# Optimization experiments

Measured on AMD Instinct MI355X. Metric: run time of the kernel, lower is better.

## Reference

```python
import jax, jax.numpy as jnp
import numpy as np

G, R, M, H, NH, OUT = 2048, 1024, 1024, 256, 8, 2
DH = H // NH


def _ln(x, g, b):
    m = jnp.mean(x, -1, keepdims=True)
    v = jnp.var(x, -1, keepdims=True)
    return (x - m) * jax.lax.rsqrt(v + 1e-5) * g + b


def _mha(xq, xkv, w, mask=None):
    # w: [4, H, H] = (Wq, Wk, Wv, Wo); mask: [Nq, Nk] bool (True = attend)
    q = (xq @ w[0]).reshape(-1, NH, DH)
    k = (xkv @ w[1]).reshape(-1, NH, DH)
    v = (xkv @ w[2]).reshape(-1, NH, DH)
    s = jnp.einsum('qhd,khd->hqk', q, k) * np.float32(1.0 / np.sqrt(DH))
    if mask is not None:
        s = jnp.where(mask[None], s, jnp.float32(-1e9))
    a = jax.nn.softmax(s, -1)
    ctx = jnp.einsum('hqk,khd->qhd', a, v).reshape(xq.shape[0], H)
    return ctx @ w[3]


def setup_inputs() -> dict:
    key = jax.random.key(0)
    ks = jax.random.split(key, 32)
    sc = np.float32(1.0 / np.sqrt(H))

    def n(i, shape, s=sc):
        return jax.random.normal(ks[i], shape, jnp.float32) * s

    inp = {}
    inp['gene_emb'] = n(0, (G, H), 0.02)
    inp['reaction_emb'] = n(1, (R, H), 0.02)
    inp['metab_emb'] = n(2, (M, H), 0.02)
    # PreProcessor (note: torch code reuses ONE LayerNorm instance -> shared params)
    inp['pre_w1'] = n(3, (H, H)); inp['pre_b1'] = jnp.zeros((H,), jnp.float32)
    inp['pre_w2'] = n(4, (H, H)); inp['pre_b2'] = jnp.zeros((H,), jnp.float32)
    inp['pre_ln_g'] = jnp.ones((H,), jnp.float32); inp['pre_ln_b'] = jnp.zeros((H,), jnp.float32)
    # NSA: 'M' block = masked attention per edge type (4), 'S' block = full self-attn per node type (3)
    inp['wm'] = n(5, (4, 4, H, H))
    inp['ws'] = n(6, (3, 4, H, H))
    inp['ln_g'] = jnp.ones((3, H), jnp.float32); inp['ln_b'] = jnp.zeros((3, H), jnp.float32)
    # AttentionalGraphAggregation
    inp['gate_w1'] = n(7, (H, H // 2)); inp['gate_b1'] = jnp.zeros((H // 2,), jnp.float32)
    inp['gate_w2'] = n(8, (H // 2, 1)); inp['gate_b2'] = jnp.zeros((1,), jnp.float32)
    inp['tr_w'] = n(9, (H, H)); inp['tr_b'] = jnp.zeros((H,), jnp.float32)
    # prediction head: num_layers=1 -> single Linear
    inp['head_w'] = n(10, (H, OUT)); inp['head_b'] = jnp.zeros((OUT,), jnp.float32)
    # dense edge masks (sparse biological graphs)
    inp['adj_pp'] = jax.random.bernoulli(ks[11], 0.01, (G, G))
    inp['adj_rr'] = jax.random.bernoulli(ks[12], 0.01, (G, G))
    inp['inc_gpr'] = jax.random.bernoulli(ks[13], 0.01, (R, G))
    inp['adj_mm'] = jax.random.bernoulli(ks[14], 0.01, (M, M))
    return inp


def reference(gene_emb, reaction_emb, metab_emb, pre_w1, pre_b1, pre_w2, pre_b2,
              pre_ln_g, pre_ln_b, wm, ws, ln_g, ln_b, gate_w1, gate_b1, gate_w2,
              gate_b2, tr_w, tr_b, head_w, head_b, adj_pp, adj_rr, inc_gpr, adj_mm):
    # preprocessor MLP on gene embeddings (single-graph path; dropout=eval/identity)
    h = jax.nn.relu(_ln(gene_emb @ pre_w1 + pre_b1, pre_ln_g, pre_ln_b))
    xg = jax.nn.relu(_ln(h @ pre_w2 + pre_b2, pre_ln_g, pre_ln_b))
    xr, xm = reaction_emb, metab_emb
    # 'M' block: masked cross/self attention per edge type, sum-aggregated per dst type
    mg = _mha(xg, xg, wm[0], adj_pp) + _mha(xg, xg, wm[1], adj_rr)
    mr = _mha(xr, xg, wm[2], inc_gpr)
    mm = _mha(xm, xm, wm[3], adj_mm)
    xg, xr, xm = xg + mg, xr + mr, xm + mm
    # 'S' block: full self-attention within each node set
    xg = xg + _mha(xg, xg, ws[0])
    xr = xr + _mha(xr, xr, ws[1])
    xm = xm + _mha(xm, xm, ws[2])
    # per-node-type layer norms (gene branch feeds the head)
    xg = _ln(xg, ln_g[0], ln_b[0])
    # attentional graph aggregation over gene nodes (single graph -> plain softmax)
    gate = jax.nn.relu(xg @ gate_w1 + gate_b1) @ gate_w2 + gate_b2  # [G, 1]
    a = jax.nn.softmax(gate, 0)
    t = jax.nn.relu(xg @ tr_w + tr_b)
    pooled = jnp.sum(a * t, 0, keepdims=True)  # [1, H]
    return pooled @ head_w + head_b  # [1, OUT]
```

## Files before the change

kernel.cpp:

```cpp
#include <hip/hip_runtime.h>
#include <hip/hip_bf16.h>
#include <cmath>
#include <cstdint>

typedef unsigned int u32;
typedef unsigned char u8;
typedef unsigned short ushort;
typedef __attribute__((ext_vector_type(8))) short short8;
typedef __attribute__((ext_vector_type(4))) float f32x4;
typedef __attribute__((ext_vector_type(16))) float f32x16;
typedef __attribute__((ext_vector_type(4))) unsigned short us4;

#define Gn 2048
#define Hd 256
#define CSTRIDE 192

static __device__ __forceinline__ ushort f2bf(float x) {
    __hip_bfloat16 b = __float2bfloat16(x);
    return *reinterpret_cast<ushort*>(&b);
}
static __device__ __forceinline__ float bf2f(ushort u) {
    return __uint_as_float(((u32)u) << 16);
}
static __device__ __forceinline__ u32 encf(float f) {
    u32 u = __float_as_uint(f);
    return u ^ (u32)(((int)u >> 31) | 0x80000000);
}
static __device__ __forceinline__ float decf(u32 u) {
    return __uint_as_float((u & 0x80000000u) ? (u ^ 0x80000000u) : ~u);
}

__global__ __launch_bounds__(256) void detect2_kernel(const u8* __restrict__ src,
                                                      int* __restrict__ cnt) {
    const int idx = blockIdx.x * 256 + threadIdx.x;
    const uint4 w = ((const uint4*)src)[idx];
    int c0 = ((w.x & 0xffu) ? 1 : 0) + ((w.y & 0xffu) ? 1 : 0) +
             ((w.z & 0xffu) ? 1 : 0) + ((w.w & 0xffu) ? 1 : 0);
    int c1 = ((w.x & 0xffffff00u) ? 1 : 0) + ((w.y & 0xffffff00u) ? 1 : 0) +
             ((w.z & 0xffffff00u) ? 1 : 0) + ((w.w & 0xffffff00u) ? 1 : 0);
    #pragma unroll
    for (int o = 1; o < 64; o <<= 1) { c0 += __shfl_xor(c0, o); c1 += __shfl_xor(c1, o); }
    if ((threadIdx.x & 63) == 0) {
        if (c0) atomicAdd(&cnt[0], c0);
        if (c1) atomicAdd(&cnt[1], c1);
    }
}

__global__ __launch_bounds__(256) void pack_mask_kernel(
    const u8* __restrict__ src0, const u8* __restrict__ src1,
    const int* __restrict__ cnt, u32* __restrict__ bits)
{
    const int z = blockIdx.y;
    const u8* src = z ? src1 : src0;
    u32* bz = bits + (long)z * 131072;
    const int idx = blockIdx.x * 256 + threadIdx.x;
    const int row = idx >> 6;
    const int w = idx & 63;
    const int f = (cnt[0] > 0) ? ((cnt[1] > 0) ? 1 : 0) : 2;
    u32 v = 0;
    if (f == 1) {
        const uint4* p = (const uint4*)(src + (long)row * 2048 + w * 32);
        const uint4 q0 = p[0], q1 = p[1];
        const u32 ws8[8] = {q0.x, q0.y, q0.z, q0.w, q1.x, q1.y, q1.z, q1.w};
        #pragma unroll
        for (int j = 0; j < 8; ++j) {
            const u32 x = ws8[j];
            const u32 m = (((x & 0x7f7f7f7fu) + 0x7f7f7f7fu) | x) & 0x80808080u;
            const u32 b4 = ((m >> 7) & 1u) | ((m >> 14) & 2u) |
                           ((m >> 21) & 4u) | ((m >> 28) & 8u);
            v |= b4 << (j * 4);
        }
    } else if (f == 0) {
        const uint4* p = (const uint4*)((const int*)src + (long)row * 2048 + w * 32);
        #pragma unroll
        for (int j = 0; j < 8; ++j) {
            const uint4 q = p[j];
            v |= (q.x ? 1u : 0u) << (j * 4 + 0);
            v |= (q.y ? 1u : 0u) << (j * 4 + 1);
            v |= (q.z ? 1u : 0u) << (j * 4 + 2);
            v |= (q.w ? 1u : 0u) << (j * 4 + 3);
        }
    } else {
        const uint4* p = (const uint4*)((const float*)src + (long)row * 2048 + w * 32);
        #pragma unroll
        for (int j = 0; j < 8; ++j) {
            const uint4 q = p[j];
            v |= ((q.x & 0x7fffffffu) ? 1u : 0u) << (j * 4 + 0);
            v |= ((q.y & 0x7fffffffu) ? 1u : 0u) << (j * 4 + 1);
            v |= ((q.z & 0x7fffffffu) ? 1u : 0u) << (j * 4 + 2);
            v |= ((q.w & 0x7fffffffu) ? 1u : 0u) << (j * 4 + 3);
        }
    }
    bz[idx] = v;
}

__global__ __launch_bounds__(256) void csr_direct_kernel(
    const u32* __restrict__ bits, int* __restrict__ deg, int* __restrict__ colidx)
{
    const int z = blockIdx.y;
    const int r = blockIdx.x * 256 + threadIdx.x;
    const u32* b = bits + (long)z * 131072 + r * 64;
    int* ci = colidx + ((long)z * 2048 + r) * CSTRIDE;
    int d = 0;
    for (int w = 0; w < 64; ++w) {
        u32 x = b[w];
        while (x) {
            const int j = __ffs(x) - 1;
            if (d < CSTRIDE) ci[d] = w * 32 + j;
            ++d;
            x &= x - 1;
        }
    }
    deg[z * 2048 + r] = d < CSTRIDE ? d : CSTRIDE;
}

__global__ __launch_bounds__(256) void preconv_kernel(
    const float* __restrict__ pre_w1, const float* __restrict__ pre_w2,
    const float* __restrict__ wm, const float* __restrict__ wsw,
    const float* __restrict__ gate_w1, const float* __restrict__ tr_w,
    ushort* __restrict__ bt_hi, ushort* __restrict__ bt_lo)
{
    const int slot = blockIdx.x;
    const int k0 = blockIdx.y * 32;
    const float* src; int ncols = 256;
    if (slot == 0) src = pre_w1;
    else if (slot == 1) src = pre_w2;
    else if (slot < 6) src = wm + (long)(slot - 2) * 65536;
    else if (slot < 10) src = wm + (long)(4 + slot - 6) * 65536;
    else if (slot < 14) src = wsw + (long)(slot - 10) * 65536;
    else if (slot == 14) { src = gate_w1; ncols = 128; }
    else src = tr_w;

    __shared__ float T[32][257];
    const int tid = threadIdx.x;
    const int lsh = (ncols == 256) ? 6 : 5;
    const int tot = 32 << lsh;
    for (int i = tid; i < tot; i += 256) {
        const int kk = i >> lsh, c4 = (i & ((1 << lsh) - 1)) << 2;
        const float4 v = *(const float4*)&src[(long)(k0 + kk) * ncols + c4];
        T[kk][c4 + 0] = v.x; T[kk][c4 + 1] = v.y;
        T[kk][c4 + 2] = v.z; T[kk][c4 + 3] = v.w;
    }
    __syncthreads();
    if (tid < ncols) {
        ushort hb[32], lb[32];
        #pragma unroll
        for (int kk = 0; kk < 32; ++kk) {
            const float x = T[kk][tid];
            const u32 bi = __float_as_uint(x);
            const ushort h = (ushort)(bi >> 16);
            const float fh = __uint_as_float(bi & 0xffff0000u);
            hb[kk] = h; lb[kk] = f2bf(x - fh);
        }
        ushort* oh = bt_hi + (long)slot * 65536 + tid * 256 + k0;
        ushort* ol = bt_lo + (long)slot * 65536 + tid * 256 + k0;
        #pragma unroll
        for (int q = 0; q < 4; ++q) {
            *(uint4*)&oh[q * 8] = *(const uint4*)&hb[q * 8];
            *(uint4*)&ol[q * 8] = *(const uint4*)&lb[q * 8];
        }
    }
}

template <int BETA, int RELU, int OUTMODE, int QKVMODE, int KT>
__global__ __launch_bounds__(128) void gemm_mfma_kernel(
    const float* __restrict__ A, int lda,
    const ushort* __restrict__ bt_hi, const ushort* __restrict__ bt_lo,
    int slot0, int slot2, const float* __restrict__ bias,
    float* __restrict__ C, int N)
{
    const int tid = threadIdx.x;
    const int wv = tid >> 6, l = tid & 63;
    const int lr = l & 15, lg = l >> 4;
    const int row = blockIdx.x * 32 + wv * 16 + lr;
    const int col0 = blockIdx.y * 64;
    int slot = slot0, zq = 0, buf = 0;
    if (QKVMODE == 1) {
        const int z = blockIdx.z;
        slot = slot0 + z + z / 3; zq = z % 3; buf = z / 3;
    } else if (QKVMODE == 2) {
        slot = slot0 + blockIdx.z; zq = blockIdx.z;
    }
    const ushort* bhb = bt_hi + (long)slot * 65536;
    const ushort* blb = bt_lo + (long)slot * 65536;
    const float* arow = A + (long)row * lda;

    const f32x4 z4 = {0.f, 0.f, 0.f, 0.f};
    f32x4 acc[4] = {z4, z4, z4, z4};

    #pragma unroll
    for (int ks = 0; ks < KT / 32; ++ks) {
        const int k0 = ks * 32;
        const ushort* bh; const ushort* bl;
        if (KT == 512 && k0 >= 256) {
            bh = bt_hi + (long)slot2 * 65536 + (k0 - 256);
            bl = bt_lo + (long)slot2 * 65536 + (k0 - 256);
        } else { bh = bhb + k0; bl = blb + k0; }
        float av[8];
        *(float4*)&av[0] = *(const float4*)&arow[k0 + lg * 8];
        *(float4*)&av[4] = *(const float4*)&arow[k0 + lg * 8 + 4];
        short8 ahi, alo;
        #pragma unroll
        for (int j = 0; j < 8; ++j) {
            const u32 bi = __float_as_uint(av[j]);
            ahi[j] = (short)(bi >> 16);
            const float fh = __uint_as_float(bi & 0xffff0000u);
            alo[j] = (short)f2bf(av[j] - fh);
        }
        #pragma unroll
        for (int f = 0; f < 4; ++f) {
            const long bo = (long)(col0 + f * 16 + lr) * 256 + lg * 8;
            const short8 bhi = *(const short8*)&bh[bo];
            const short8 blo = *(const short8*)&bl[bo];
            acc[f] = __builtin_amdgcn_mfma_f32_16x16x32_bf16(ahi, bhi, acc[f], 0, 0, 0);
            acc[f] = __builtin_amdgcn_mfma_f32_16x16x32_bf16(alo, bhi, acc[f], 0, 0, 0);
            acc[f] = __builtin_amdgcn_mfma_f32_16x16x32_bf16(ahi, blo, acc[f], 0, 0, 0);
        }
    }

    const float QS = 0.17677669529663687f * 1.4426950408889634f;

    #pragma unroll
    for (int f = 0; f < 4; ++f) {
        const int col = col0 + f * 16 + lr;
        const float bv = bias ? bias[col] : 0.f;
        #pragma unroll
        for (int r = 0; r < 4; ++r) {
            const int rr = blockIdx.x * 32 + wv * 16 + lg * 4 + r;
            float v = acc[f][r] + bv;
            if (OUTMODE == 1) {
                if (zq == 0) v *= QS;
                ushort* ob = (ushort*)C + (long)buf * 1572864;
                const int h = col >> 5, d = col & 31;
                if (QKVMODE == 1 || zq < 2)
                    ob[zq * 524288 + ((h * 2048 + rr) << 5) + d] = f2bf(v);
                else
                    ob[1048576 + ((h * 32 + d) << 11) + rr] = f2bf(v);
            } else {
                if (BETA) v += C[(long)rr * N + col];
                if (RELU) v = fmaxf(v, 0.f);
                C[(long)rr * N + col] = v;
            }
        }
    }
}

template <int RELU, int DUP>
__global__ __launch_bounds__(64) void ln_kernel(
    const float* __restrict__ X, const float* __restrict__ gw,
    const float* __restrict__ bw, float* __restrict__ Y, float* __restrict__ Y2)
{
    const int row = blockIdx.x, tid = threadIdx.x;
    const float4 x = *(const float4*)&X[(long)row * 256 + (tid << 2)];
    float s = x.x + x.y + x.z + x.w;
    float s2 = x.x * x.x + x.y * x.y + x.z * x.z + x.w * x.w;
    #pragma unroll
    for (int o = 1; o < 64; o <<= 1) { s += __shfl_xor(s, o); s2 += __shfl_xor(s2, o); }
    const float mean = s * (1.f / 256.f);
    const float var = s2 * (1.f / 256.f) - mean * mean;
    const float rs = rsqrtf(var + 1e-5f);
    const float4 g4 = *(const float4*)&gw[tid << 2];
    const float4 b4 = *(const float4*)&bw[tid << 2];
    float4 y;
    y.x = (x.x - mean) * rs * g4.x + b4.x;
    y.y = (x.y - mean) * rs * g4.y + b4.y;
    y.z = (x.z - mean) * rs * g4.z + b4.z;
    y.w = (x.w - mean) * rs * g4.w + b4.w;
    if (RELU) {
        y.x = fmaxf(y.x, 0.f); y.y = fmaxf(y.y, 0.f);
        y.z = fmaxf(y.z, 0.f); y.w = fmaxf(y.w, 0.f);
    }
    *(float4*)&Y[(long)row * 256 + (tid << 2)] = y;
    if (DUP) *(float4*)&Y2[(long)row * 256 + (tid << 2)] = y;
}

__global__ __launch_bounds__(64) void attn_sparse_kernel(
    const ushort* __restrict__ qkvb, const int* __restrict__ deg,
    const int* __restrict__ colidx, float* __restrict__ ctx)
{
    const int r = blockIdx.x, z = blockIdx.y;
    const ushort* qb = qkvb + (long)z * 1572864;
    const ushort* kb = qb + 524288;
    const ushort* vr = qb + 1048576;
    const int l = threadIdx.x;
    const int h = l >> 3, dg = l & 7;
    float* orow = &ctx[(long)r * 512 + z * 256 + h * 32 + dg * 4];
    const int n = deg[z * 2048 + r];
    if (n == 0) {
        float a0 = 0.f, a1 = 0.f, a2 = 0.f, a3 = 0.f;
        for (int k = 0; k < 2048; ++k) {
            const us4 vv = *(const us4*)&vr[((h * 2048 + k) << 5) + dg * 4];
            a0 += bf2f(vv[0]); a1 += bf2f(vv[1]); a2 += bf2f(vv[2]); a3 += bf2f(vv[3]);
        }
        float4 o; const float inv = 1.f / 2048.f;
        o.x = a0 * inv; o.y = a1 * inv; o.z = a2 * inv; o.w = a3 * inv;
        *(float4*)orow = o;
        return;
    }
    float q0, q1, q2, q3;
    {
        const us4 qv = *(const us4*)&qb[((h * 2048 + r) << 5) + dg * 4];
        q0 = bf2f(qv[0]); q1 = bf2f(qv[1]); q2 = bf2f(qv[2]); q3 = bf2f(qv[3]);
    }
    const int* ci = colidx + ((long)z * 2048 + r) * CSTRIDE;
    float m = -INFINITY, lsum = 0.f;
    float a0 = 0.f, a1 = 0.f, a2 = 0.f, a3 = 0.f;
    int kn = ci[0];
    us4 kv = *(const us4*)&kb[((h * 2048 + kn) << 5) + dg * 4];
    us4 vv = *(const us4*)&vr[((h * 2048 + kn) << 5) + dg * 4];
    for (int e = 0; e < n; ++e) {
        const us4 kc = kv, vc = vv;
        if (e + 1 < n) {
            kn = ci[e + 1];
            kv = *(const us4*)&kb[((h * 2048 + kn) << 5) + dg * 4];
            vv = *(const us4*)&vr[((h * 2048 + kn) << 5) + dg * 4];
        }
        float s = q0 * bf2f(kc[0]) + q1 * bf2f(kc[1]) +
                  q2 * bf2f(kc[2]) + q3 * bf2f(kc[3]);
        s += __shfl_xor(s, 1); s += __shfl_xor(s, 2); s += __shfl_xor(s, 4);
        const float mn = fmaxf(m, s);
        const float fac = __builtin_amdgcn_exp2f(m - mn);
        const float p = __builtin_amdgcn_exp2f(s - mn);
        lsum = lsum * fac + p;
        a0 = a0 * fac + p * bf2f(vc[0]);
        a1 = a1 * fac + p * bf2f(vc[1]);
        a2 = a2 * fac + p * bf2f(vc[2]);
// ... 80 lines not shown
        asm volatile("v_permlane32_swap_b32 %0, %1" : "+v"(pk[4]), "+v"(pk[6]));
        asm volatile("v_permlane32_swap_b32 %0, %1" : "+v"(pk[5]), "+v"(pk[7]));
        short8 pB0, pB1;
        ((u32*)&pB0)[0] = pk[0]; ((u32*)&pB0)[1] = pk[1];
        ((u32*)&pB0)[2] = pk[2]; ((u32*)&pB0)[3] = pk[3];
        ((u32*)&pB1)[0] = pk[4]; ((u32*)&pB1)[1] = pk[5];
        ((u32*)&pB1)[2] = pk[6]; ((u32*)&pB1)[3] = pk[7];
        const int voff = ((h * 32 + lq) << 11) + kbase + hi * 8;
        const short8 vf0 = *(const short8*)&vt[voff];
        const short8 vf1 = *(const short8*)&vt[voff + 16];
        acc = __builtin_amdgcn_mfma_f32_32x32x16_bf16(vf0, pB0, acc, 0, 0, 0);
        acc = __builtin_amdgcn_mfma_f32_32x32x16_bf16(vf1, pB1, acc, 0, 0, 0);
    }

    if (wv) {
        if (l < 32) { Mm[wv - 1][l] = m; Ml[wv - 1][l] = lsum; }
        #pragma unroll
        for (int i = 0; i < 16; ++i) Macc[wv - 1][l][i] = acc[i];
    }
    __syncthreads();
    if (wv == 0) {
        float M = m;
        #pragma unroll
        for (int w = 0; w < 7; ++w) M = fmaxf(M, Mm[w][lq]);
        const float f0 = __builtin_amdgcn_exp2f(m - M);
        float den = lsum * f0;
        float o[16];
        #pragma unroll
        for (int i = 0; i < 16; ++i) o[i] = acc[i] * f0;
        #pragma unroll
        for (int w = 0; w < 7; ++w) {
            const float fw = __builtin_amdgcn_exp2f(Mm[w][lq] - M);
            den += Ml[w][lq] * fw;
            #pragma unroll
            for (int i = 0; i < 16; ++i) o[i] += Macc[w][l][i] * fw;
        }
        const float inv = 1.f / den;
        #pragma unroll
        for (int i = 0; i < 16; ++i)
            ctile[(i & 3) + 8 * (i >> 2) + 4 * hi][lq] = o[i] * inv;
    }
    __syncthreads();
    if (threadIdx.x < 256) {
        const int t = threadIdx.x;
        const int q = t >> 3, d0 = (t & 7) << 2;
        float4 ov;
        ov.x = ctile[d0 + 0][q]; ov.y = ctile[d0 + 1][q];
        ov.z = ctile[d0 + 2][q]; ov.w = ctile[d0 + 3][q];
        *(float4*)&ctx[(long)(qt * 32 + q) * 512 + h * 32 + d0] = ov;
    }
}

__global__ __launch_bounds__(64) void aggr_gemm_kernel(
    const float* __restrict__ xg,
    const ushort* __restrict__ bt_hi, const ushort* __restrict__ bt_lo,
    const float* __restrict__ tr_b, const float* __restrict__ g_b1,
    const float* __restrict__ g_w2, const float* __restrict__ g_b2,
    float* __restrict__ t_out, float* __restrict__ gv, u32* __restrict__ gmax)
{
    const int l = threadIdx.x;
    const int lr = l & 15, lg = l >> 4;
    const int row0 = blockIdx.x * 16;
    const int gate = (blockIdx.y == 8);
    const int slot = gate ? 14 : 15;
    const int col0 = gate ? 0 : blockIdx.y * 32;
    const int NF = gate ? 8 : 2;
    const ushort* bh0 = bt_hi + (long)slot * 65536;
    const ushort* bl0 = bt_lo + (long)slot * 65536;
    const float* arow = xg + (long)(row0 + lr) * 256;

    const f32x4 z4 = {0.f, 0.f, 0.f, 0.f};
    f32x4 acc[8] = {z4, z4, z4, z4, z4, z4, z4, z4};

    #pragma unroll
    for (int ks = 0; ks < 8; ++ks) {
        const int k0 = ks * 32;
        float av[8];
        *(float4*)&av[0] = *(const float4*)&arow[k0 + lg * 8];
        *(float4*)&av[4] = *(const float4*)&arow[k0 + lg * 8 + 4];
        short8 ahi, alo;
        #pragma unroll
        for (int j = 0; j < 8; ++j) {
            const u32 bi = __float_as_uint(av[j]);
            ahi[j] = (short)(bi >> 16);
            const float fh = __uint_as_float(bi & 0xffff0000u);
            alo[j] = (short)f2bf(av[j] - fh);
        }
        for (int f = 0; f < NF; ++f) {
            const long bo = (long)(col0 + f * 16 + lr) * 256 + k0 + lg * 8;
            const short8 bhi = *(const short8*)&bh0[bo];
            const short8 blo = *(const short8*)&bl0[bo];
            acc[f] = __builtin_amdgcn_mfma_f32_16x16x32_bf16(ahi, bhi, acc[f], 0, 0, 0);
            acc[f] = __builtin_amdgcn_mfma_f32_16x16x32_bf16(alo, bhi, acc[f], 0, 0, 0);
            acc[f] = __builtin_amdgcn_mfma_f32_16x16x32_bf16(ahi, blo, acc[f], 0, 0, 0);
        }
    }

    if (!gate) {
        #pragma unroll
        for (int f = 0; f < 2; ++f) {
            const int col = col0 + f * 16 + lr;
            const float bv = tr_b[col];
            #pragma unroll
            for (int r = 0; r < 4; ++r) {
                const int rr = row0 + lg * 4 + r;
                t_out[(long)rr * 256 + col] = fmaxf(acc[f][r] + bv, 0.f);
            }
        }
    } else {
        float b1v[8], w2v[8];
        #pragma unroll
        for (int f = 0; f < 8; ++f) {
            b1v[f] = g_b1[f * 16 + lr];
            w2v[f] = g_w2[f * 16 + lr];
        }
        const float b2 = g_b2[0];
        #pragma unroll
        for (int r = 0; r < 4; ++r) {
            float t = 0.f;
            #pragma unroll
            for (int f = 0; f < 8; ++f)
                t += fmaxf(acc[f][r] + b1v[f], 0.f) * w2v[f];
            #pragma unroll
            for (int o = 1; o < 16; o <<= 1) t += __shfl_xor(t, o);
            if (lr == 0) {
                const float g = t + b2;
                gv[row0 + lg * 4 + r] = g;
                atomicMax(gmax, encf(g));
            }
        }
    }
}

__global__ __launch_bounds__(256) void wsum_part_kernel(
    const float* __restrict__ gv, const u32* __restrict__ gmax,
    const float* __restrict__ t, float* __restrict__ partial,
    float* __restrict__ denp)
{
    const float L2E = 1.4426950408889634f;
    const int b = blockIdx.x, tid = threadIdx.x;
    const float M = decf(*gmax);
    float s = 0.f, den = 0.f;
    #pragma unroll 4
    for (int i = 0; i < 32; ++i) {
        const int r = b * 32 + i;
        const float w = __builtin_amdgcn_exp2f((gv[r] - M) * L2E);
        den += w;
        s += w * t[(long)r * 256 + tid];
    }
    partial[b * 256 + tid] = s;
    if (tid == 0) denp[b] = den;
}

__global__ __launch_bounds__(256) void head2_kernel(
    const float* __restrict__ partial, const float* __restrict__ denp,
    const float* __restrict__ hw, const float* __restrict__ hb,
    float* __restrict__ out)
{
    __shared__ float red0[4], red1[4];
    const int tid = threadIdx.x;
    float p = 0.f;
    #pragma unroll 8
    for (int b = 0; b < 64; ++b) p += partial[b * 256 + tid];
    float den = 0.f;
    #pragma unroll
    for (int b = 0; b < 64; ++b) den += denp[b];
    p /= den;
    float s0 = p * hw[tid * 2 + 0];
    float s1 = p * hw[tid * 2 + 1];
    #pragma unroll
    for (int o = 1; o < 64; o <<= 1) { s0 += __shfl_xor(s0, o); s1 += __shfl_xor(s1, o); }
    if ((tid & 63) == 0) { red0[tid >> 6] = s0; red1[tid >> 6] = s1; }
    __syncthreads();
    if (tid == 0) {
        out[0] = red0[0] + red0[1] + red0[2] + red0[3] + hb[0];
        out[1] = red1[0] + red1[1] + red1[2] + red1[3] + hb[1];
    }
}

extern "C" void kernel_launch(void* const* d_in, const int* in_sizes, int n_in,
                              void* d_out, int out_size, void* d_ws, size_t ws_size,
                              hipStream_t stream)
{
    (void)in_sizes; (void)n_in; (void)out_size; (void)ws_size;
    const float* gene_emb = (const float*)d_in[0];
    const float* pre_w1   = (const float*)d_in[3];
    const float* pre_b1   = (const float*)d_in[4];
    const float* pre_w2   = (const float*)d_in[5];
    const float* pre_b2   = (const float*)d_in[6];
    const float* pre_ln_g = (const float*)d_in[7];
    const float* pre_ln_b = (const float*)d_in[8];
    const float* wm       = (const float*)d_in[9];
    const float* wsw      = (const float*)d_in[10];
    const float* ln_g     = (const float*)d_in[11];
    const float* ln_b     = (const float*)d_in[12];
    const float* gate_w1  = (const float*)d_in[13];
    const float* gate_b1  = (const float*)d_in[14];
    const float* gate_w2  = (const float*)d_in[15];
    const float* gate_b2  = (const float*)d_in[16];
    const float* tr_w     = (const float*)d_in[17];
    const float* tr_b     = (const float*)d_in[18];
    const float* head_w   = (const float*)d_in[19];
    const float* head_b   = (const float*)d_in[20];
    const u8* adj_pp      = (const u8*)d_in[21];
    const u8* adj_rr      = (const u8*)d_in[22];

    const long NHf = (long)Gn * Hd;
    float* tmp0    = (float*)d_ws;
    float* xg      = tmp0 + NHf;
    float* xg1     = xg + NHf;
    float* ctx2    = xg1 + NHf;
    float* gv      = ctx2 + 2 * NHf;
    float* partial = gv + Gn;
    float* denp    = partial + 64 * 256;
    int* cnt       = (int*)(denp + 64);
    int* deg       = cnt + 64;
    int* colidx    = deg + 4096;
    u32* bits      = (u32*)(colidx + 2L * 2048 * CSTRIDE);
    ushort* qkvb   = (ushort*)(bits + 262144);
    ushort* bt_hi  = qkvb + 2L * 1572864;
    ushort* bt_lo  = bt_hi + 16L * 65536;

    dim3 B256(256), T64(64), B128(128);
    dim3 gS(64, 4);

    hipMemsetAsync((void*)cnt, 0, 16, stream);
    detect2_kernel<<<dim3(64), B256, 0, stream>>>(adj_pp, cnt);
    pack_mask_kernel<<<dim3(512, 2), B256, 0, stream>>>(adj_pp, adj_rr, cnt, bits);
    csr_direct_kernel<<<dim3(8, 2), B256, 0, stream>>>(bits, deg, colidx);
    preconv_kernel<<<dim3(16, 8), B256, 0, stream>>>(pre_w1, pre_w2, wm, wsw,
                                                     gate_w1, tr_w, bt_hi, bt_lo);

    gemm_mfma_kernel<0, 0, 0, 0, 256><<<gS, B128, 0, stream>>>(gene_emb, 256, bt_hi, bt_lo, 0, 0, pre_b1, tmp0, 256);
    ln_kernel<1, 0><<<dim3(2048), T64, 0, stream>>>(tmp0, pre_ln_g, pre_ln_b, xg, nullptr);
    gemm_mfma_kernel<0, 0, 0, 0, 256><<<gS, B128, 0, stream>>>(xg, 256, bt_hi, bt_lo, 1, 0, pre_b2, tmp0, 256);
    ln_kernel<1, 1><<<dim3(2048), T64, 0, stream>>>(tmp0, pre_ln_g, pre_ln_b, xg, xg1);

    gemm_mfma_kernel<0, 0, 1, 1, 256><<<dim3(64, 4, 6), B128, 0, stream>>>(xg, 256, bt_hi, bt_lo, 2, 0, nullptr, (float*)qkvb, 256);
    attn_sparse_kernel<<<dim3(2048, 2), T64, 0, stream>>>(qkvb, deg, colidx, ctx2);
    gemm_mfma_kernel<1, 0, 0, 0, 512><<<gS, B128, 0, stream>>>(ctx2, 512, bt_hi, bt_lo, 5, 9, nullptr, xg1, 256);

    gemm_mfma_kernel<0, 0, 1, 2, 256><<<dim3(64, 4, 3), B128, 0, stream>>>(xg1, 256, bt_hi, bt_lo, 10, 0, nullptr, (float*)qkvb, 256);
    attn_dense_kernel<<<dim3(8, 64), dim3(512), 0, stream>>>(qkvb, ctx2);
    gemm_mfma_kernel<1, 0, 0, 0, 256><<<gS, B128, 0, stream>>>(ctx2, 512, bt_hi, bt_lo, 13, 0, nullptr, xg1, 256);
    ln_kernel<0, 0><<<dim3(2048), T64, 0, stream>>>(xg1, ln_g, ln_b, xg, nullptr);

    aggr_gemm_kernel<<<dim3(128, 9), T64, 0, stream>>>(xg, bt_hi, bt_lo, tr_b, gate_b1, gate_w2, gate_b2, tmp0, gv, (u32*)&cnt[2]);
    wsum_part_kernel<<<dim3(64), B256, 0, stream>>>(gv, (const u32*)&cnt[2], tmp0, partial, denp);
    head2_kernel<<<dim3(1), B256, 0, stream>>>(partial, denp, head_w, head_b, (float*)d_out);
}
```

Baseline: 227.0 us.

## Merge preprocessing kernels and fuse layer norms into GEMM prologues

Combines mask detection with weight conversion, and mask packing with the first GEMM, into merged kernels that use disjoint block ranges. Each separate LayerNorm pass is folded into the consuming GEMM's A-load, which recomputes row statistics per block. The global atomic max for the gate softmax is replaced by per-block maxima that are rescaled in the head kernel, which also removes the memset. The aim is to cut launch count and intermediate round-trips, at the cost of redundant LN statistics work and heavier heterogeneous kernels.

```diff
diff --git a/kernel.cpp b/kernel.cpp
--- a/kernel.cpp
+++ b/kernel.cpp
@@ -22,168 +22,44 @@
 static __device__ __forceinline__ float bf2f(ushort u) {
     return __uint_as_float(((u32)u) << 16);
 }
-static __device__ __forceinline__ u32 encf(float f) {
-    u32 u = __float_as_uint(f);
-    return u ^ (u32)(((int)u >> 31) | 0x80000000);
-}
-static __device__ __forceinline__ float decf(u32 u) {
-    return __uint_as_float((u & 0x80000000u) ? (u ^ 0x80000000u) : ~u);
-}
-
-__global__ __launch_bounds__(256) void detect2_kernel(const u8* __restrict__ src,
-                                                      int* __restrict__ cnt) {
-    const int idx = blockIdx.x * 256 + threadIdx.x;
-    const uint4 w = ((const uint4*)src)[idx];
-    int c0 = ((w.x & 0xffu) ? 1 : 0) + ((w.y & 0xffu) ? 1 : 0) +
-             ((w.z & 0xffu) ? 1 : 0) + ((w.w & 0xffu) ? 1 : 0);
-    int c1 = ((w.x & 0xffffff00u) ? 1 : 0) + ((w.y & 0xffffff00u) ? 1 : 0) +
-             ((w.z & 0xffffff00u) ? 1 : 0) + ((w.w & 0xffffff00u) ? 1 : 0);
-    #pragma unroll
-    for (int o = 1; o < 64; o <<= 1) { c0 += __shfl_xor(c0, o); c1 += __shfl_xor(c1, o); }
-    if ((threadIdx.x & 63) == 0) {
-        if (c0) atomicAdd(&cnt[0], c0);
-        if (c1) atomicAdd(&cnt[1], c1);
-    }
-}
-
-__global__ __launch_bounds__(256) void pack_mask_kernel(
-    const u8* __restrict__ src0, const u8* __restrict__ src1,
-    const int* __restrict__ cnt, u32* __restrict__ bits)
-{
-    const int z = blockIdx.y;
-    const u8* src = z ? src1 : src0;
-    u32* bz = bits + (long)z * 131072;
-    const int idx = blockIdx.x * 256 + threadIdx.x;
-    const int row = idx >> 6;
-    const int w = idx & 63;
-    const int f = (cnt[0] > 0) ? ((cnt[1] > 0) ? 1 : 0) : 2;
-    u32 v = 0;
-    if (f == 1) {
-        const uint4* p = (const uint4*)(src + (long)row * 2048 + w * 32);
-        const uint4 q0 = p[0], q1 = p[1];
-        const u32 ws8[8] = {q0.x, q0.y, q0.z, q0.w, q1.x, q1.y, q1.z, q1.w};
-        #pragma unroll
-        for (int j = 0; j < 8; ++j) {
-            const u32 x = ws8[j];
-            const u32 m = (((x & 0x7f7f7f7fu) + 0x7f7f7f7fu) | x) & 0x80808080u;
-            const u32 b4 = ((m >> 7) & 1u) | ((m >> 14) & 2u) |
-                           ((m >> 21) & 4u) | ((m >> 28) & 8u);
-            v |= b4 << (j * 4);
-        }
-    } else if (f == 0) {
-        const uint4* p = (const uint4*)((const int*)src + (long)row * 2048 + w * 32);
-        #pragma unroll
-        for (int j = 0; j < 8; ++j) {
-            const uint4 q = p[j];
-            v |= (q.x ? 1u : 0u) << (j * 4 + 0);
-            v |= (q.y ? 1u : 0u) << (j * 4 + 1);
-            v |= (q.z ? 1u : 0u) << (j * 4 + 2);
-            v |= (q.w ? 1u : 0u) << (j * 4 + 3);
-        }
-    } else {
-        const uint4* p = (const uint4*)((const float*)src + (long)row * 2048 + w * 32);
-        #pragma unroll
-        for (int j = 0; j < 8; ++j) {
-            const uint4 q = p[j];
-            v |= ((q.x & 0x7fffffffu) ? 1u : 0u) << (j * 4 + 0);
-            v |= ((q.y & 0x7fffffffu) ? 1u : 0u) << (j * 4 + 1);
-            v |= ((q.z & 0x7fffffffu) ? 1u : 0u) << (j * 4 + 2);
-            v |= ((q.w & 0x7fffffffu) ? 1u : 0u) << (j * 4 + 3);
-        }
-    }
-    bz[idx] = v;
-}
-
-__global__ __launch_bounds__(256) void csr_direct_kernel(
-    const u32* __restrict__ bits, int* __restrict__ deg, int* __restrict__ colidx)
-{
-    const int z = blockIdx.y;
-    const int r = blockIdx.x * 256 + threadIdx.x;
-    const u32* b = bits + (long)z * 131072 + r * 64;
-    int* ci = colidx + ((long)z * 2048 + r) * CSTRIDE;
-    int d = 0;
-    for (int w = 0; w < 64; ++w) {
-        u32 x = b[w];
-        while (x) {
-            const int j = __ffs(x) - 1;
-            if (d < CSTRIDE) ci[d] = w * 32 + j;
-            ++d;
-            x &= x - 1;
-        }
-    }
-    deg[z * 2048 + r] = d < CSTRIDE ? d : CSTRIDE;
-}
-
-__global__ __launch_bounds__(256) void preconv_kernel(
-    const float* __restrict__ pre_w1, const float* __restrict__ pre_w2,
-    const float* __restrict__ wm, const float* __restrict__ wsw,
-    const float* __restrict__ gate_w1, const float* __restrict__ tr_w,
-    ushort* __restrict__ bt_hi, ushort* __restrict__ bt_lo)
-{
-    const int slot = blockIdx.x;
-    const int k0 = blockIdx.y * 32;
-    const float* src; int ncols = 256;
-    if (slot == 0) src = pre_w1;
-    else if (slot == 1) src = pre_w2;
-    else if (slot < 6) src = wm + (long)(slot - 2) * 65536;
-    else if (slot < 10) src = wm + (long)(4 + slot - 6) * 65536;
-    else if (slot < 14) src = wsw + (long)(slot - 10) * 65536;
-    else if (slot == 14) { src = gate_w1; ncols = 128; }
-    else src = tr_w;
-
-    __shared__ float T[32][257];
-    const int tid = threadIdx.x;
-    const int lsh = (ncols == 256) ? 6 : 5;
-    const int tot = 32 << lsh;
-    for (int i = tid; i < tot; i += 256) {
-        const int kk = i >> lsh, c4 = (i & ((1 << lsh) - 1)) << 2;
-        const float4 v = *(const float4*)&src[(long)(k0 + kk) * ncols + c4];
-        T[kk][c4 + 0] = v.x; T[kk][c4 + 1] = v.y;
-        T[kk][c4 + 2] = v.z; T[kk][c4 + 3] = v.w;
-    }
-    __syncthreads();
-    if (tid < ncols) {
-        ushort hb[32], lb[32];
-        #pragma unroll
-        for (int kk = 0; kk < 32; ++kk) {
-            const float x = T[kk][tid];
-            const u32 bi = __float_as_uint(x);
-            const ushort h = (ushort)(bi >> 16);
-            const float fh = __uint_as_float(bi & 0xffff0000u);
-            hb[kk] = h; lb[kk] = f2bf(x - fh);
-        }
-        ushort* oh = bt_hi + (long)slot * 65536 + tid * 256 + k0;
-        ushort* ol = bt_lo + (long)slot * 65536 + tid * 256 + k0;
-        #pragma unroll
-        for (int q = 0; q < 4; ++q) {
-            *(uint4*)&oh[q * 8] = *(const uint4*)&hb[q * 8];
-            *(uint4*)&ol[q * 8] = *(const uint4*)&lb[q * 8];
-        }
-    }
-}
-
-template <int BETA, int RELU, int OUTMODE, int QKVMODE, int KT>
-__global__ __launch_bounds__(128) void gemm_mfma_kernel(
+
+template <int BETA, int OUTMODE, int QKVMODE, int KT, int LNF, int LNRELU, int WRA>
+static __device__ __forceinline__ void gemm_body(
+    const int bx, const int by, const int bz,
     const float* __restrict__ A, int lda,
     const ushort* __restrict__ bt_hi, const ushort* __restrict__ bt_lo,
     int slot0, int slot2, const float* __restrict__ bias,
-    float* __restrict__ C, int N)
+    const float* __restrict__ lng, const float* __restrict__ lnb,
+    float* __restrict__ C, int N, float* __restrict__ Aout)
 {
     const int tid = threadIdx.x;
     const int wv = tid >> 6, l = tid & 63;
     const int lr = l & 15, lg = l >> 4;
-    const int row = blockIdx.x * 32 + wv * 16 + lr;
-    const int col0 = blockIdx.y * 64;
+    const int row = bx * 32 + wv * 16 + lr;
+    const int col0 = by * 64;
     int slot = slot0, zq = 0, buf = 0;
-    if (QKVMODE == 1) {
-        const int z = blockIdx.z;
-        slot = slot0 + z + z / 3; zq = z % 3; buf = z / 3;
-    } else if (QKVMODE == 2) {
-        slot = slot0 + blockIdx.z; zq = blockIdx.z;
-    }
+    if (QKVMODE == 1) { slot = slot0 + bz + bz / 3; zq = bz % 3; buf = bz / 3; }
+    else if (QKVMODE == 2) { slot = slot0 + bz; zq = bz; }
     const ushort* bhb = bt_hi + (long)slot * 65536;
     const ushort* blb = bt_lo + (long)slot * 65536;
     const float* arow = A + (long)row * lda;
+
+    float mean = 0.f, rs = 0.f;
+    if (LNF) {
+        float s = 0.f, s2 = 0.f;
+        #pragma unroll
+        for (int ks = 0; ks < 8; ++ks) {
+            const float4 a0 = *(const float4*)&arow[ks * 32 + lg * 8];
+            const float4 a1 = *(const float4*)&arow[ks * 32 + lg * 8 + 4];
+            s  += (a0.x + a0.y) + (a0.z + a0.w) + (a1.x + a1.y) + (a1.z + a1.w);
+            s2 += a0.x * a0.x + a0.y * a0.y + a0.z * a0.z + a0.w * a0.w +
+                  a1.x * a1.x + a1.y * a1.y + a1.z * a1.z + a1.w * a1.w;
+        }
+        s += __shfl_xor(s, 16);  s += __shfl_xor(s, 32);
+        s2 += __shfl_xor(s2, 16); s2 += __shfl_xor(s2, 32);
+        mean = s * (1.f / 256.f);
+        rs = rsqrtf(s2 * (1.f / 256.f) - mean * mean + 1e-5f);
+    }
 
     const f32x4 z4 = {0.f, 0.f, 0.f, 0.f};
     f32x4 acc[4] = {z4, z4, z4, z4};
@@ -199,6 +75,23 @@
         float av[8];
         *(float4*)&av[0] = *(const float4*)&arow[k0 + lg * 8];
         *(float4*)&av[4] = *(const float4*)&arow[k0 + lg * 8 + 4];
+        if (LNF) {
+            float gvv[8], bvv[8];
+            *(float4*)&gvv[0] = *(const float4*)&lng[k0 + lg * 8];
+            *(float4*)&gvv[4] = *(const float4*)&lng[k0 + lg * 8 + 4];
+            *(float4*)&bvv[0] = *(const float4*)&lnb[k0 + lg * 8];
+            *(float4*)&bvv[4] = *(const float4*)&lnb[k0 + lg * 8 + 4];
+            #pragma unroll
+            for (int j = 0; j < 8; ++j) {
+                float v = (av[j] - mean) * rs * gvv[j] + bvv[j];
+                if (LNRELU) v = fmaxf(v, 0.f);
+                av[j] = v;
+            }
+            if (WRA && by == 0 && bz == 0) {
+                *(float4*)&Aout[(long)row * 256 + k0 + lg * 8] = *(float4*)&av[0];
+                *(float4*)&Aout[(long)row * 256 + k0 + lg * 8 + 4] = *(float4*)&av[4];
+            }
+        }
         short8 ahi, alo;
         #pragma unroll
         for (int j = 0; j < 8; ++j) {
@@ -226,7 +119,7 @@
         const float bv = bias ? bias[col] : 0.f;
         #pragma unroll
         for (int r = 0; r < 4; ++r) {
-            const int rr = blockIdx.x * 32 + wv * 16 + lg * 4 + r;
+            const int rr = bx * 32 + wv * 16 + lg * 4 + r;
             float v = acc[f][r] + bv;
             if (OUTMODE == 1) {
                 if (zq == 0) v *= QS;
@@ -238,40 +131,210 @@
                     ob[1048576 + ((h * 32 + d) << 11) + rr] = f2bf(v);
             } else {
                 if (BETA) v += C[(long)rr * N + col];
-                if (RELU) v = fmaxf(v, 0.f);
                 C[(long)rr * N + col] = v;
             }
         }
     }
 }
 
-template <int RELU, int DUP>
-__global__ __launch_bounds__(64) void ln_kernel(
-    const float* __restrict__ X, const float* __restrict__ gw,
-    const float* __restrict__ bw, float* __restrict__ Y, float* __restrict__ Y2)
-{
-    const int row = blockIdx.x, tid = threadIdx.x;
-    const float4 x = *(const float4*)&X[(long)row * 256 + (tid << 2)];
-    float s = x.x + x.y + x.z + x.w;
-    float s2 = x.x * x.x + x.y * x.y + x.z * x.z + x.w * x.w;
-    #pragma unroll
-    for (int o = 1; o < 64; o <<= 1) { s += __shfl_xor(s, o); s2 += __shfl_xor(s2, o); }
-    const float mean = s * (1.f / 256.f);
-    const float var = s2 * (1.f / 256.f) - mean * mean;
-    const float rs = rsqrtf(var + 1e-5f);
-    const float4 g4 = *(const float4*)&gw[tid << 2];
-    const float4 b4 = *(const float4*)&bw[tid << 2];
-    float4 y;
-    y.x = (x.x - mean) * rs * g4.x + b4.x;
-    y.y = (x.y - mean) * rs * g4.y + b4.y;
-    y.z = (x.z - mean) * rs * g4.z + b4.z;
-    y.w = (x.w - mean) * rs * g4.w + b4.w;
-    if (RELU) {
-        y.x = fmaxf(y.x, 0.f); y.y = fmaxf(y.y, 0.f);
-        y.z = fmaxf(y.z, 0.f); y.w = fmaxf(y.w, 0.f);
-    }
-    *(float4*)&Y[(long)row * 256 + (tid << 2)] = y;
-    if (DUP) *(float4*)&Y2[(long)row * 256 + (tid << 2)] = y;
+__global__ __launch_bounds__(256) void mergedA_kernel(
+    const u8* __restrict__ adj, int* __restrict__ det0, int* __restrict__ det1,
+    const float* __restrict__ pre_w1, const float* __restrict__ pre_w2,
+    const float* __restrict__ wm, const float* __restrict__ wsw,
+    const float* __restrict__ gate_w1, const float* __restrict__ tr_w,
+    ushort* __restrict__ bt_hi, ushort* __restrict__ bt_lo)
+{
+    __shared__ float T[32][257];
+    __shared__ int sd0[4], sd1[4];
+    const int tid = threadIdx.x;
+    if (blockIdx.x < 64) {
+        const int idx = blockIdx.x * 256 + tid;
+        const uint4 w = ((const uint4*)adj)[idx];
+        int c0 = ((w.x & 0xffu) ? 1 : 0) + ((w.y & 0xffu) ? 1 : 0) +
+                 ((w.z & 0xffu) ? 1 : 0) + ((w.w & 0xffu) ? 1 : 0);
+        int c1 = ((w.x & 0xffffff00u) ? 1 : 0) + ((w.y & 0xffffff00u) ? 1 : 0) +
+                 ((w.z & 0xffffff00u) ? 1 : 0) + ((w.w & 0xffffff00u) ? 1 : 0);
+        #pragma unroll
+        for (int o = 1; o < 64; o <<= 1) { c0 += __shfl_xor(c0, o); c1 += __shfl_xor(c1, o); }
+        if ((tid & 63) == 0) { sd0[tid >> 6] = c0; sd1[tid >> 6] = c1; }
+        __syncthreads();
+        if (tid == 0) {
+            det0[blockIdx.x] = sd0[0] + sd0[1] + sd0[2] + sd0[3];
+            det1[blockIdx.x] = sd1[0] + sd1[1] + sd1[2] + sd1[3];
+        }
+        return;
+    }
+    const int b2 = blockIdx.x - 64;
+    const int slot = b2 >> 3;
+    const int k0 = (b2 & 7) * 32;
+    const float* src; int ncols = 256;
+    if (slot == 0) src = pre_w1;
+    else if (slot == 1) src = pre_w2;
+    else if (slot < 6) src = wm + (long)(slot - 2) * 65536;
+    else if (slot < 10) src = wm + (long)(4 + slot - 6) * 65536;
+    else if (slot < 14) src = wsw + (long)(slot - 10) * 65536;
+    else if (slot == 14) { src = gate_w1; ncols = 128; }
+    else src = tr_w;
+
+    const int lsh = (ncols == 256) ? 6 : 5;
+    const int tot = 32 << lsh;
+    for (int i = tid; i < tot; i += 256) {
+        const int kk = i >> lsh, c4 = (i & ((1 << lsh) - 1)) << 2;
+        const float4 v = *(const float4*)&src[(long)(k0 + kk) * ncols + c4];
+        T[kk][c4 + 0] = v.x; T[kk][c4 + 1] = v.y;
+        T[kk][c4 + 2] = v.z; T[kk][c4 + 3] = v.w;
+    }
+    __syncthreads();
+    if (tid < ncols) {
+        ushort hb[32], lb[32];
+        #pragma unroll
+        for (int kk = 0; kk < 32; ++kk) {
+            const float x = T[kk][tid];
+            const u32 bi = __float_as_uint(x);
+            const ushort h = (ushort)(bi >> 16);
+            const float fh = __uint_as_float(bi & 0xffff0000u);
+            hb[kk] = h; lb[kk] = f2bf(x - fh);
+        }
+        ushort* oh = bt_hi + (long)slot * 65536 + tid * 256 + k0;
+        ushort* ol = bt_lo + (long)slot * 65536 + tid * 256 + k0;
+        #pragma unroll
+        for (int q = 0; q < 4; ++q) {
+            *(uint4*)&oh[q * 8] = *(const uint4*)&hb[q * 8];
+            *(uint4*)&ol[q * 8] = *(const uint4*)&lb[q * 8];
+        }
+    }
+}
+
+__global__ __launch_bounds__(128) void mergedB_kernel(
+    const u8* __restrict__ src0, const u8* __restrict__ src1,
+    const int* __restrict__ det0, const int* __restrict__ det1,
+    u32* __restrict__ bits,
+    const float* __restrict__ gene_emb,
+    const ushort* __restrict__ bt_hi, const ushort* __restrict__ bt_lo,
+    const float* __restrict__ pre_b1, float* __restrict__ tmp0)
+{
+    const int tid = threadIdx.x;
+    if (blockIdx.x < 2048) {
+        const int lane = tid & 63;
+        int c0 = det0[lane], c1 = det1[lane];
+        #pragma unroll
+        for (int o = 1; o < 64; o <<= 1) { c0 += __shfl_xor(c0, o); c1 += __shfl_xor(c1, o); }
+        const int f = (c0 > 0) ? ((c1 > 0) ? 1 : 0) : 2;
+        const int W = blockIdx.x * 128 + tid;
+        const int z = W >> 17;
+        const int rem = W & 131071;
+        const int row = rem >> 6, w = rem & 63;
+        const u8* src = z ? src1 : src0;
+        u32 v = 0;
+        if (f == 1) {
+            const uint4* p = (const uint4*)(src + (long)row * 2048 + w * 32);
+            const uint4 q0 = p[0], q1 = p[1];
+            const u32 ws8[8] = {q0.x, q0.y, q0.z, q0.w, q1.x, q1.y, q1.z, q1.w};
+            #pragma unroll
+            for (int j = 0; j < 8; ++j) {
+                const u32 x = ws8[j];
+                const u32 m = (((x & 0x7f7f7f7fu) + 0x7f7f7f7fu) | x) & 0x80808080u;
+                const u32 b4 = ((m >> 7) & 1u) | ((m >> 14) & 2u) |
+                               ((m >> 21) & 4u) | ((m >> 28) & 8u);
+                v |= b4 << (j * 4);
+            }
+        } else if (f == 0) {
+            const uint4* p = (const uint4*)((const int*)src + (long)row * 2048 + w * 32);
+            #pragma unroll
+            for (int j = 0; j < 8; ++j) {
+                const uint4 q = p[j];
+                v |= (q.x ? 1u : 0u) << (j * 4 + 0);
+                v |= (q.y ? 1u : 0u) << (j * 4 + 1);
+                v |= (q.z ? 1u : 0u) << (j * 4 + 2);
+                v |= (q.w ? 1u : 0u) << (j * 4 + 3);
+            }
+        } else {
+            const uint4* p = (const uint4*)((const float*)src + (long)row * 2048 + w * 32);
+            #pragma unroll
+            for (int j = 0; j < 8; ++j) {
+                const uint4 q = p[j];
+                v |= ((q.x & 0x7fffffffu) ? 1u : 0u) << (j * 4 + 0);
+                v |= ((q.y & 0x7fffffffu) ? 1u : 0u) << (j * 4 + 1);
+                v |= ((q.z & 0x7fffffffu) ? 1u : 0u) << (j * 4 + 2);
+                v |= ((q.w & 0x7fffffffu) ? 1u : 0u) << (j * 4 + 3);
+            }
+        }
+        bits[(long)z * 131072 + rem] = v;
+        return;
+    }
+    const int b2 = blockIdx.x - 2048;
+    gemm_body<0, 0, 0, 256, 0, 0, 0>(b2 >> 2, b2 & 3, 0, gene_emb, 256,
+                                     bt_hi, bt_lo, 0, 0, pre_b1,
+                                     nullptr, nullptr, tmp0, 256, nullptr);
+}
+
+__global__ __launch_bounds__(128) void mergedC_kernel(
+    const u32* __restrict__ bits, int* __restrict__ deg, int* __restrict__ colidx,
+    const float* __restrict__ tmp0,
+    const ushort* __restrict__ bt_hi, const ushort* __restrict__ bt_lo,
+    const float* __restrict__ pre_b2, const float* __restrict__ pre_ln_g,
+    const float* __restrict__ pre_ln_b, float* __restrict__ tmp1)
+{
+    if (blockIdx.x < 32) {
+        const int flat = blockIdx.x * 128 + threadIdx.x;
+        const int z = flat >> 11, r = flat & 2047;
+        const u32* b = bits + (long)z * 131072 + r * 64;
+        int* ci = colidx + ((long)z * 2048 + r) * CSTRIDE;
+        int d = 0;
+        for (int w = 0; w < 64; ++w) {
+            u32 x = b[w];
+            while (x) {
+                const int j = __ffs(x) - 1;
+                if (d < CSTRIDE) ci[d] = w * 32 + j;
+                ++d;
+                x &= x - 1;
+            }
+        }
+        deg[z * 2048 + r] = d < CSTRIDE ? d : CSTRIDE;
+        return;
+    }
+    const int b2 = blockIdx.x - 32;
+    gemm_body<0, 0, 0, 256, 1, 1, 0>(b2 >> 2, b2 & 3, 0, tmp0, 256,
+                                     bt_hi, bt_lo, 1, 0, pre_b2,
+                                     pre_ln_g, pre_ln_b, tmp1, 256, nullptr);
+}
+
+__global__ __launch_bounds__(128) void qkvm_kernel(
+    const float* __restrict__ tmp1,
+    const ushort* __restrict__ bt_hi, const ushort* __restrict__ bt_lo,
+    const float* __restrict__ pre_ln_g, const float* __restrict__ pre_ln_b,
+    float* __restrict__ qkvb, float* __restrict__ xg1)
+{
+    gemm_body<0, 1, 1, 256, 1, 1, 1>(blockIdx.x, blockIdx.y, blockIdx.z,
+                                     tmp1, 256, bt_hi, bt_lo, 2, 0, nullptr,
+                                     pre_ln_g, pre_ln_b, qkvb, 256, xg1);
+}
+__global__ __launch_bounds__(128) void wo_m_kernel(
+    const float* __restrict__ ctx2,
+    const ushort* __restrict__ bt_hi, const ushort* __restrict__ bt_lo,
+    float* __restrict__ xg1)
+{
+    gemm_body<1, 0, 0, 512, 0, 0, 0>(blockIdx.x, blockIdx.y, 0, ctx2, 512,
+                                     bt_hi, bt_lo, 5, 9, nullptr,
+                                     nullptr, nullptr, xg1, 256, nullptr);
+}
+__global__ __launch_bounds__(128) void qkvs_kernel(
+    const float* __restrict__ xg1,
+    const ushort* __restrict__ bt_hi, const ushort* __restrict__ bt_lo,
+    float* __restrict__ qkvb)
+{
+    gemm_body<0, 1, 2, 256, 0, 0, 0>(blockIdx.x, blockIdx.y, blockIdx.z,
+                                     xg1, 256, bt_hi, bt_lo, 10, 0, nullptr,
+                                     nullptr, nullptr, qkvb, 256, nullptr);
+}
+__global__ __launch_bounds__(128) void wo_s_kernel(
+    const float* __restrict__ ctx2,
+    const ushort* __restrict__ bt_hi, const ushort* __restrict__ bt_lo,
+    float* __restrict__ xg1)
+{
+    gemm_body<1, 0, 0, 256, 0, 0, 0>(blockIdx.x, blockIdx.y, 0, ctx2, 512,
+                                     bt_hi, bt_lo, 13, 0, nullptr,
+                                     nullptr, nullptr, xg1, 256, nullptr);
 }
 
 __global__ __launch_bounds__(64) void attn_sparse_kernel(
@@ -458,11 +521,12 @@
 }
 
 __global__ __launch_bounds__(64) void aggr_gemm_kernel(
-    const float* __restrict__ xg,
+    const float* __restrict__ xg1,
     const ushort* __restrict__ bt_hi, const ushort* __restrict__ bt_lo,
+    const float* __restrict__ ln_g, const float* __restrict__ ln_b,
     const float* __restrict__ tr_b, const float* __restrict__ g_b1,
     const float* __restrict__ g_w2, const float* __restrict__ g_b2,
-    float* __restrict__ t_out, float* __restrict__ gv, u32* __restrict__ gmax)
+    float* __restrict__ t_out, float* __restrict__ gv)
 {
     const int l = threadIdx.x;
     const int lr = l & 15, lg = l >> 4;
@@ -473,7 +537,21 @@
     const int NF = gate ? 8 : 2;
     const ushort* bh0 = bt_hi + (long)slot * 65536;
     const ushort* bl0 = bt_lo + (long)slot * 65536;
-    const float* arow = xg + (long)(row0 + lr) * 256;
+    const float* arow = xg1 + (long)(row0 + lr) * 256;
+
+    float s = 0.f, s2 = 0.f;
+    #pragma unroll
+    for (int ks = 0; ks < 8; ++ks) {
+        const float4 a0 = *(const float4*)&arow[ks * 32 + lg * 8];
+        const float4 a1 = *(const float4*)&arow[ks * 32 + lg * 8 + 4];
+        s  += (a0.x + a0.y) + (a0.z + a0.w) + (a1.x + a1.y) + (a1.z + a1.w);
+        s2 += a0.x * a0.x + a0.y * a0.y + a0.z * a0.z + a0.w * a0.w +
+              a1.x * a1.x + a1.y * a1.y + a1.z * a1.z + a1.w * a1.w;
+    }
+    s += __shfl_xor(s, 16);  s += __shfl_xor(s, 32);
+    s2 += __shfl_xor(s2, 16); s2 += __shfl_xor(s2, 32);
+    const float mean = s * (1.f / 256.f);
+    const float rs = rsqrtf(s2 * (1.f / 256.f) - mean * mean + 1e-5f);
 
     const f32x4 z4 = {0.f, 0.f, 0.f, 0.f};
     f32x4 acc[8] = {z4, z4, z4, z4, z4, z4, z4, z4};
@@ -481,16 +559,21 @@
     #pragma unroll
     for (int ks = 0; ks < 8; ++ks) {
         const int k0 = ks * 32;
-        float av[8];
+        float av[8], gvv[8], bvv[8];
         *(float4*)&av[0] = *(const float4*)&arow[k0 + lg * 8];
         *(float4*)&av[4] = *(const float4*)&arow[k0 + lg * 8 + 4];
+        *(float4*)&gvv[0] = *(const float4*)&ln_g[k0 + lg * 8];
+        *(float4*)&gvv[4] = *(const float4*)&ln_g[k0 + lg * 8 + 4];
+        *(float4*)&bvv[0] = *(const float4*)&ln_b[k0 + lg * 8];
+        *(float4*)&bvv[4] = *(const float4*)&ln_b[k0 + lg * 8 + 4];
         short8 ahi, alo;
         #pragma unroll
         for (int j = 0; j < 8; ++j) {
-            const u32 bi = __float_as_uint(av[j]);
+            const float vn = (av[j] - mean) * rs * gvv[j] + bvv[j];
+            const u32 bi = __float_as_uint(vn);
             ahi[j] = (short)(bi >> 16);
             const float fh = __uint_as_float(bi & 0xffff0000u);
-            alo[j] = (short)f2bf(av[j] - fh);
+            alo[j] = (short)f2bf(vn - fh);
         }
         for (int f = 0; f < NF; ++f) {
             const long bo = (long)(col0 + f * 16 + lr) * 256 + k0 + lg * 8;
@@ -529,23 +612,20 @@
                 t += fmaxf(acc[f][r] + b1v[f], 0.f) * w2v[f];
             #pragma unroll
             for (int o = 1; o < 16; o <<= 1) t += __shfl_xor(t, o);
-            if (lr == 0) {
-                const float g = t + b2;
-                gv[row0 + lg * 4 + r] = g;
-                atomicMax(gmax, encf(g));
-            }
+            if (lr == 0) gv[row0 + lg * 4 + r] = t + b2;
         }
     }
 }
 
 __global__ __launch_bounds__(256) void wsum_part_kernel(
-    const float* __restrict__ gv, const u32* __restrict__ gmax,
-    const float* __restrict__ t, float* __restrict__ partial,
-    float* __restrict__ denp)
+    const float* __restrict__ gv, const float* __restrict__ t,
+    float* __restrict__ partial, float* __restrict__ denp, float* __restrict__ mpart)
 {
     const float L2E = 1.4426950408889634f;
     const int b = blockIdx.x, tid = threadIdx.x;
-    const float M = decf(*gmax);
+    float M = -INFINITY;
+    #pragma unroll
+    for (int i = 0; i < 32; ++i) M = fmaxf(M, gv[b * 32 + i]);
     float s = 0.f, den = 0.f;
     #pragma unroll 4
     for (int i = 0; i < 32; ++i) {
@@ -555,23 +635,36 @@
         s += w * t[(long)r * 256 + tid];
     }
     partial[b * 256 + tid] = s;
-    if (tid == 0) denp[b] = den;
+    if (tid == 0) { denp[b] = den; mpart[b] = M; }
 }
 
 __global__ __launch_bounds__(256) void head2_kernel(
     const float* __restrict__ partial, const float* __restrict__ denp,
-    const float* __restrict__ hw, const float* __restrict__ hb,
-    float* __restrict__ out)
-{
+    const float* __restrict__ mpart, const float* __restrict__ hw,
+    const float* __restrict__ hb, float* __restrict__ out)
+{
+    __shared__ float fb[64];
+    __shared__ float dtot;
     __shared__ float red0[4], red1[4];
+    const float L2E = 1.4426950408889634f;
     const int tid = threadIdx.x;
+    if (tid < 64) {
+        const float mb = mpart[tid];
+        float M = mb;
+        #pragma unroll
+        for (int o = 1; o < 64; o <<= 1) M = fmaxf(M, __shfl_xor(M, o));
+        const float f = __builtin_amdgcn_exp2f((mb - M) * L2E);
+        fb[tid] = f;
+        float dv = f * denp[tid];
+        #pragma unroll
+        for (int o = 1; o < 64; o <<= 1) dv += __shfl_xor(dv, o);
+        if (tid == 0) dtot = dv;
+    }
+    __syncthreads();
     float p = 0.f;
     #pragma unroll 8
-    for (int b = 0; b < 64; ++b) p += partial[b * 256 + tid];
-    float den = 0.f;
-    #pragma unroll
-    for (int b = 0; b < 64; ++b) den += denp[b];
-    p /= den;
+    for (int b = 0; b < 64; ++b) p += fb[b] * partial[b * 256 + tid];
+    p /= dtot;
     float s0 = p * hw[tid * 2 + 0];
     float s1 = p * hw[tid * 2 + 1];
     #pragma unroll
@@ -613,45 +706,39 @@
 
     const long NHf = (long)Gn * Hd;
     float* tmp0    = (float*)d_ws;
-    float* xg      = tmp0 + NHf;
-    float* xg1     = xg + NHf;
+    float* tmp1    = tmp0 + NHf;
+    float* xg1     = tmp1 + NHf;
     float* ctx2    = xg1 + NHf;
     float* gv      = ctx2 + 2 * NHf;
     float* partial = gv + Gn;
     float* denp    = partial + 64 * 256;
-    int* cnt       = (int*)(denp + 64);
-    int* deg       = cnt + 64;
+    float* mpart   = denp + 64;
+    int* det0      = (int*)(mpart + 64);
+    int* det1      = det0 + 64;
+    int* deg       = det1 + 64;
     int* colidx    = deg + 4096;
     u32* bits      = (u32*)(colidx + 2L * 2048 * CSTRIDE);
     ushort* qkvb   = (ushort*)(bits + 262144);
     ushort* bt_hi  = qkvb + 2L * 1572864;
     ushort* bt_lo  = bt_hi + 16L * 65536;
 
-    dim3 B256(256), T64(64), B128(128);
-    dim3 gS(64, 4);
-
-    hipMemsetAsync((void*)cnt, 0, 16, stream);
-    detect2_kernel<<<dim3(64), B256, 0, stream>>>(adj_pp, cnt);
-    pack_mask_kernel<<<dim3(512, 2), B256, 0, stream>>>(adj_pp, adj_rr, cnt, bits);
-    csr_direct_kernel<<<dim3(8, 2), B256, 0, stream>>>(bits, deg, colidx);
-    preconv_kernel<<<dim3(16, 8), B256, 0, stream>>>(pre_w1, pre_w2, wm, wsw,
-                                                     gate_w1, tr_w, bt_hi, bt_lo);
-
-    gemm_mfma_kernel<0, 0, 0, 0, 256><<<gS, B128, 0, stream>>>(gene_emb, 256, bt_hi, bt_lo, 0, 0, pre_b1, tmp0, 256);
-    ln_kernel<1, 0><<<dim3(2048), T64, 0, stream>>>(tmp0, pre_ln_g, pre_ln_b, xg, nullptr);
-    gemm_mfma_kernel<0, 0, 0, 0, 256><<<gS, B128, 0, stream>>>(xg, 256, bt_hi, bt_lo, 1, 0, pre_b2, tmp0, 256);
-    ln_kernel<1, 1><<<dim3(2048), T64, 0, stream>>>(tmp0, pre_ln_g, pre_ln_b, xg, xg1);
-
-    gemm_mfma_kernel<0, 0, 1, 1, 256><<<dim3(64, 4, 6), B128, 0, stream>>>(xg, 256, bt_hi, bt_lo, 2, 0, nullptr, (float*)qkvb, 256);
+    dim3 B256(256), B128(128), T64(64);
+
+    mergedA_kernel<<<dim3(192), B256, 0, stream>>>(adj_pp, det0, det1,
+        pre_w1, pre_w2, wm, wsw, gate_w1, tr_w, bt_hi, bt_lo);
+    mergedB_kernel<<<dim3(2304), B128, 0, stream>>>(adj_pp, adj_rr, det0, det1,
+        bits, gene_emb, bt_hi, bt_lo, pre_b1, tmp0);
+    mergedC_kernel<<<dim3(288), B128, 0, stream>>>(bits, deg, colidx, tmp0,
+        bt_hi, bt_lo, pre_b2, pre_ln_g, pre_ln_b, tmp1);
+    qkvm_kernel<<<dim3(64, 4, 6), B128, 0, stream>>>(tmp1, bt_hi, bt_lo,
+        pre_ln_g, pre_ln_b, (float*)qkvb, xg1);
     attn_sparse_kernel<<<dim3(2048, 2), T64, 0, stream>>>(qkvb, deg, colidx, ctx2);
-    gemm_mfma_kernel<1, 0, 0, 0, 512><<<gS, B128, 0, stream>>>(ctx2, 512, bt_hi, bt_lo, 5, 9, nullptr, xg1, 256);
-
-    gemm_mfma_kernel<0, 0, 1, 2, 256><<<dim3(64, 4, 3), B128, 0, stream>>>(xg1, 256, bt_hi, bt_lo, 10, 0, nullptr, (float*)qkvb, 256);
+    wo_m_kernel<<<dim3(64, 4), B128, 0, stream>>>(ctx2, bt_hi, bt_lo, xg1);
+    qkvs_kernel<<<dim3(64, 4, 3), B128, 0, stream>>>(xg1, bt_hi, bt_lo, (float*)qkvb);
     attn_dense_kernel<<<dim3(8, 64), dim3(512), 0, stream>>>(qkvb, ctx2);
-    gemm_mfma_kernel<1, 0, 0, 0, 256><<<gS, B128, 0, stream>>>(ctx2, 512, bt_hi, bt_lo, 13, 0, nullptr, xg1, 256);
-    ln_kernel<0, 0><<<dim3(2048), T64, 0, stream>>>(xg1, ln_g, ln_b, xg, nullptr);
-
-    aggr_gemm_kernel<<<dim3(128, 9), T64, 0, stream>>>(xg, bt_hi, bt_lo, tr_b, gate_b1, gate_w2, gate_b2, tmp0, gv, (u32*)&cnt[2]);
-    wsum_part_kernel<<<dim3(64), B256, 0, stream>>>(gv, (const u32*)&cnt[2], tmp0, partial, denp);
-    head2_kernel<<<dim3(1), B256, 0, stream>>>(partial, denp, head_w, head_b, (float*)d_out);
-}
+    wo_s_kernel<<<dim3(64, 4), B128, 0, stream>>>(ctx2, bt_hi, bt_lo, xg1);
+    aggr_gemm_kernel<<<dim3(128, 9), T64, 0, stream>>>(xg1, bt_hi, bt_lo,
+        ln_g, ln_b, tr_b, gate_b1, gate_w2, gate_b2, tmp0, gv);
+    wsum_part_kernel<<<dim3(64), B256, 0, stream>>>(gv, tmp0, partial, denp, mpart);
+    head2_kernel<<<dim3(1), B256, 0, stream>>>(partial, denp, mpart, head_w, head_b, (float*)d_out);
+}
```

Measured after the change: 204.2 us. -10.0%, faster.
